# Performance work log

Measured on AMD Instinct MI355X. Metric: run time of the kernel, lower is better.

## Reference

```python
import jax, jax.numpy as jnp
import numpy as np

DIM = 64          # d_model
D_INNER = 128     # 2 * DIM (mamba expand=2)
D_STATE = 16
D_CONV = 4
DT_RANK = 4       # ceil(DIM / 16)


def setup_inputs() -> dict:
    key = jax.random.key(0)
    ks = jax.random.split(key, 8)
    s = 0.05
    f32 = jnp.float32
    return {
        "x": jax.random.normal(ks[0], (2, DIM, 96, 96), f32),
        # GroupNorm(1, dim)
        "gn_gamma": jnp.ones((DIM,), f32),
        "gn_beta": jnp.zeros((DIM,), f32),
        # Mamba params
        "W_in": (jax.random.normal(ks[1], (2 * D_INNER, DIM), f32) * s),
        "b_in": jnp.zeros((2 * D_INNER,), f32),
        "conv_w": (jax.random.normal(ks[2], (D_INNER, 1, D_CONV), f32) * s),
        "conv_b": jnp.zeros((D_INNER,), f32),
        "W_xproj": (jax.random.normal(ks[3], (DT_RANK + 2 * D_STATE, D_INNER), f32) * s),
        "W_dt": (jax.random.normal(ks[4], (D_INNER, DT_RANK), f32) * s),
        "b_dt": jnp.full((D_INNER,), -4.6, f32),  # softplus(-4.6) ~ 0.01
        "A_log": jnp.log(jnp.broadcast_to(jnp.arange(1, D_STATE + 1, dtype=f32), (D_INNER, D_STATE))),
        "Dp": jnp.ones((D_INNER,), f32),
        "W_out": (jax.random.normal(ks[5], (DIM, D_INNER), f32) * s),
        "b_out": jnp.zeros((DIM,), f32),
        # proj: Conv2d(dim, dim, 1) + BatchNorm2d(dim) eval-mode + GELU
        "proj_w": (jax.random.normal(ks[6], (DIM, DIM), f32) * s),
        "proj_b": jnp.zeros((DIM,), f32),
        "bn_gamma": jnp.ones((DIM,), f32),
        "bn_beta": jnp.zeros((DIM,), f32),
        "bn_mean": jnp.zeros((DIM,), f32),
        "bn_var": jnp.ones((DIM,), f32),
    }


def _mamba(u, W_in, b_in, conv_w, conv_b, W_xproj, W_dt, b_dt, A_log, Dp, W_out, b_out):
    # u: [B, L, DIM]
    xz = u @ W_in.T + b_in                      # [B, L, 2*D_INNER]
    x, z = jnp.split(xz, 2, axis=-1)            # each [B, L, D_INNER]
    # depthwise causal conv over L
    xc = jnp.transpose(x, (0, 2, 1))            # [B, D_INNER, L]
    xc = jax.lax.conv_general_dilated(
        xc, conv_w, (1,), [(D_CONV - 1, 0)],
        dimension_numbers=("NCH", "OIH", "NCH"), feature_group_count=D_INNER)
    x = jax.nn.silu(jnp.transpose(xc, (0, 2, 1)) + conv_b)   # [B, L, D_INNER]
    # input-dependent dt, B, C
    dbc = x @ W_xproj.T                          # [B, L, DT_RANK + 2*D_STATE]
    dt = dbc[..., :DT_RANK]
    Bm = dbc[..., DT_RANK:DT_RANK + D_STATE]     # [B, L, D_STATE]
    Cm = dbc[..., DT_RANK + D_STATE:]            # [B, L, D_STATE]
    dt = jax.nn.softplus(dt @ W_dt.T + b_dt)     # [B, L, D_INNER]
    A = -jnp.exp(A_log)                          # [D_INNER, D_STATE]
    deltaA = jnp.exp(dt[..., None] * A)                          # [B, L, D_INNER, D_STATE]
    deltaBu = dt[..., None] * Bm[:, :, None, :] * x[..., None]   # [B, L, D_INNER, D_STATE]
    # parallel linear recurrence h_t = a_t * h_{t-1} + b_t, h_0 = 0
    def comb(e1, e2):
        a1, b1 = e1
        a2, b2 = e2
        return a1 * a2, a2 * b1 + b2
    _, h = jax.lax.associative_scan(comb, (deltaA, deltaBu), axis=1)
    y = jnp.einsum("blds,bls->bld", h, Cm) + x * Dp
    y = y * jax.nn.silu(z)
    return y @ W_out.T + b_out                   # [B, L, DIM]


def reference(x, gn_gamma, gn_beta, W_in, b_in, conv_w, conv_b, W_xproj, W_dt, b_dt,
              A_log, Dp, W_out, b_out, proj_w, proj_b, bn_gamma, bn_beta, bn_mean, bn_var):
    B, C, H, W = x.shape
    # GroupNorm(1, C): normalize over (C, H, W) per sample, biased var
    mu = x.mean(axis=(1, 2, 3), keepdims=True)
    var = x.var(axis=(1, 2, 3), keepdims=True)
    xn = (x - mu) / jnp.sqrt(var + 1e-5)
    xn = xn * gn_gamma[None, :, None, None] + gn_beta[None, :, None, None]
    xn = jnp.clip(xn, -10.0, 10.0)
    res = xn
    seq = jnp.transpose(xn, (0, 2, 3, 1)).reshape(B, H * W, C)
    y = _mamba(seq, W_in, b_in, conv_w, conv_b, W_xproj, W_dt, b_dt, A_log, Dp, W_out, b_out)
    y2d = jnp.transpose(y.reshape(B, H, W, C), (0, 3, 1, 2))
    # proj: 1x1 conv + eval BatchNorm + exact GELU
    p = jnp.einsum("oc,bchw->bohw", proj_w, y2d) + proj_b[None, :, None, None]
    p = (p - bn_mean[None, :, None, None]) / jnp.sqrt(bn_var[None, :, None, None] + 1e-5)
    p = p * bn_gamma[None, :, None, None] + bn_beta[None, :, None, None]
    p = jax.nn.gelu(p, approximate=False)
    return jnp.clip(res + p, -10.0, 10.0)
```

## Files before the change

kernel.cpp:

```cpp
#include <hip/hip_runtime.h>
#include <math.h>

#define DIMC 64
#define DIN  128
#define LSEQ 9216
#define NPB  (DIMC*LSEQ)
#define NCH  192
#define CTL  48
#define NCHAIN 4096

__device__ __forceinline__ float siluf(float v)    { return v / (1.f + __expf(-v)); }
__device__ __forceinline__ float softplusf(float v){ return (v > 15.f) ? v : __logf(1.f + __expf(v)); }
__device__ __forceinline__ float clip10(float v)   { return fminf(10.f, fmaxf(-10.f, v)); }

__global__ void k_reduce(const float* __restrict__ x, float* __restrict__ sums) {
  int b = blockIdx.y;
  const float* xb = x + (size_t)b * NPB;
  float s = 0.f, s2 = 0.f;
  for (int i = blockIdx.x * blockDim.x + threadIdx.x; i < NPB; i += gridDim.x * blockDim.x) {
    float v = xb[i]; s += v; s2 = fmaf(v, v, s2);
  }
  __shared__ float l1[256], l2[256];
  int t = threadIdx.x;
  l1[t] = s; l2[t] = s2; __syncthreads();
  for (int off = 128; off > 0; off >>= 1) {
    if (t < off) { l1[t] += l1[t + off]; l2[t] += l2[t + off]; }
    __syncthreads();
  }
  if (t == 0) { atomicAdd(&sums[2*b], l1[0]); atomicAdd(&sums[2*b+1], l2[0]); }
}

__global__ void k_norm(const float* __restrict__ x, const float* __restrict__ gam,
                       const float* __restrict__ bet, const float* __restrict__ sums,
                       float* __restrict__ seq, float* __restrict__ res) {
  int b = blockIdx.y, l0 = blockIdx.x * 64;
  float mean = sums[2*b] * (1.f / NPB);
  float var  = sums[2*b+1] * (1.f / NPB) - mean * mean;
  float inv  = rsqrtf(var + 1e-5f);
  __shared__ float tile[64][65];
  int t = threadIdx.x;
  int lr = t & 63, cg = t >> 6;
  #pragma unroll
  for (int i = 0; i < 16; i++) {
    int c = i * 4 + cg;
    size_t idx = ((size_t)(b * DIMC + c)) * LSEQ + l0 + lr;
    float v = x[idx];
    v = (v - mean) * inv * gam[c] + bet[c];
    v = clip10(v);
    res[idx] = v;
    tile[c][lr] = v;
  }
  __syncthreads();
  int cc = t & 63, lg = t >> 6;
  #pragma unroll
  for (int i = 0; i < 16; i++) {
    int l = i * 4 + lg;
    seq[((size_t)(b * LSEQ + l0 + l)) * DIMC + cc] = tile[cc][l];
  }
}

__global__ void k_prep(const float* __restrict__ W_in, const float* __restrict__ proj_w,
                       const float* __restrict__ W_out, const float* __restrict__ b_out,
                       const float* __restrict__ proj_b, const float* __restrict__ W_xproj,
                       const float* __restrict__ W_dt,
                       float* __restrict__ Wt, float* __restrict__ Mt, float* __restrict__ bp,
                       float* __restrict__ Wbtd, float* __restrict__ Wbc) {
  int i = blockIdx.x * 256 + threadIdx.x;
  if (i < 16384) {
    int k = i >> 8, c = i & 255;
    Wt[i] = W_in[c * 64 + k];
    return;
  }
  int j = i - 16384;
  if (j < 8192) {
    int d = j >> 6, o = j & 63;
    float a = 0.f;
    for (int c = 0; c < 64; c++) a = fmaf(proj_w[o * 64 + c], W_out[c * DIN + d], a);
    Mt[j] = a;
    return;
  }
  int k2 = j - 8192;
  if (k2 < 64) {
    float a = proj_b[k2];
    for (int c = 0; c < 64; c++) a = fmaf(proj_w[k2 * 64 + c], b_out[c], a);
    bp[k2] = a;
    return;
  }
  int m = j - 8256;
  if (m < 16384) {
    int k = m >> 7, c = m & 127;
    float v = 0.f;
    #pragma unroll
    for (int r = 0; r < 4; r++) v = fmaf(W_dt[c * 4 + r], W_xproj[r * DIN + k], v);
    Wbtd[m] = v;
    return;
  }
  int m2 = m - 16384;
  if (m2 < 4096) {
    int k = m2 >> 5, jj = m2 & 31;
    Wbc[m2] = W_xproj[(4 + jj) * DIN + k];
  }
}

__global__ void __launch_bounds__(256) k_mid(
    const float* __restrict__ seq, const float* __restrict__ Wt,
    const float* __restrict__ b_in, const float* __restrict__ conv_w,
    const float* __restrict__ conv_b, const float* __restrict__ Wbtd,
    const float* __restrict__ Wbc, const float* __restrict__ b_dt,
    float* __restrict__ xs, float* __restrict__ zo, float* __restrict__ dt,
    float* __restrict__ Bm, float* __restrict__ Cm) {
  int row0 = blockIdx.x * 16;
  int l0 = row0 % LSEQ;
  int t = threadIdx.x;
  __shared__ float sq[19 * 64];
  __shared__ float xt[16 * DIN];
  for (int i = t; i < 19 * 16; i += 256) {
    int r = i >> 4, k4 = i & 15;
    int rr = row0 - 3 + r; if (rr < 0) rr = 0;
    *(float4*)(sq + r * 64 + k4 * 4) = *(const float4*)(seq + (size_t)rr * DIMC + k4 * 4);
  }
  __syncthreads();

  {
    int c = t;
    float bi = b_in[c];
    float a[19];
    #pragma unroll
    for (int r = 0; r < 19; r++) a[r] = bi;
    const float4* sq4 = (const float4*)sq;
    #pragma unroll 4
    for (int k4 = 0; k4 < 16; k4++) {
      float w0 = Wt[(k4 * 4 + 0) * 256 + c];
      float w1 = Wt[(k4 * 4 + 1) * 256 + c];
      float w2 = Wt[(k4 * 4 + 2) * 256 + c];
      float w3 = Wt[(k4 * 4 + 3) * 256 + c];
      #pragma unroll
      for (int r = 0; r < 19; r++) {
        float4 v = sq4[r * 16 + k4];
        a[r] = fmaf(w0, v.x, a[r]);
        a[r] = fmaf(w1, v.y, a[r]);
        a[r] = fmaf(w2, v.z, a[r]);
        a[r] = fmaf(w3, v.w, a[r]);
      }
    }
    if (c < DIN) {
      if (l0 == 0) { a[0] = 0.f; a[1] = 0.f; a[2] = 0.f; }
      float4 cw = *(const float4*)(conv_w + c * 4);
      float cb = conv_b[c];
      #pragma unroll
      for (int i = 0; i < 16; i++) {
        float v = cb;
        v = fmaf(a[i + 0], cw.x, v);
        v = fmaf(a[i + 1], cw.y, v);
        v = fmaf(a[i + 2], cw.z, v);
        v = fmaf(a[i + 3], cw.w, v);
        float sv = siluf(v);
        xs[(size_t)(row0 + i) * DIN + c] = sv;
        xt[i * DIN + c] = sv;
      }
    } else {
      int cz = c - DIN;
      #pragma unroll
      for (int i = 0; i < 16; i++) zo[(size_t)(row0 + i) * DIN + cz] = a[i + 3];
    }
  }
  __syncthreads();

  {
    int cd = t & 127, rb = (t >> 7) * 8;
    float acc[8];
    float bb = b_dt[cd];
    #pragma unroll
    for (int r = 0; r < 8; r++) acc[r] = bb;
    const float4* xt4 = (const float4*)(xt + rb * DIN);
    #pragma unroll 2
    for (int k4 = 0; k4 < 32; k4++) {
      float w0 = Wbtd[(k4 * 4 + 0) * 128 + cd];
      float w1 = Wbtd[(k4 * 4 + 1) * 128 + cd];
      float w2 = Wbtd[(k4 * 4 + 2) * 128 + cd];
      float w3 = Wbtd[(k4 * 4 + 3) * 128 + cd];
      #pragma unroll
      for (int r = 0; r < 8; r++) {
        float4 v = xt4[r * 32 + k4];
        acc[r] = fmaf(w0, v.x, acc[r]);
        acc[r] = fmaf(w1, v.y, acc[r]);
        acc[r] = fmaf(w2, v.z, acc[r]);
        acc[r] = fmaf(w3, v.w, acc[r]);
      }
    }
    #pragma unroll
    for (int r = 0; r < 8; r++)
      dt[(size_t)(row0 + rb + r) * DIN + cd] = softplusf(acc[r]);
  }

  {
    int cb = t & 31, rg = t >> 5;
    float a0 = 0.f, a1 = 0.f;
    const float4* x0 = (const float4*)(xt + (rg * 2 + 0) * DIN);
    const float4* x1 = (const float4*)(xt + (rg * 2 + 1) * DIN);
    #pragma unroll 2
    for (int k4 = 0; k4 < 32; k4++) {
      float w0 = Wbc[(k4 * 4 + 0) * 32 + cb];
      float w1 = Wbc[(k4 * 4 + 1) * 32 + cb];
      float w2 = Wbc[(k4 * 4 + 2) * 32 + cb];
      float w3 = Wbc[(k4 * 4 + 3) * 32 + cb];
      float4 v0 = x0[k4], v1 = x1[k4];
      a0 = fmaf(w0, v0.x, a0); a0 = fmaf(w1, v0.y, a0);
      a0 = fmaf(w2, v0.z, a0); a0 = fmaf(w3, v0.w, a0);
      a1 = fmaf(w0, v1.x, a1); a1 = fmaf(w1, v1.y, a1);
      a1 = fmaf(w2, v1.z, a1); a1 = fmaf(w3, v1.w, a1);
    }
    size_t r0 = (size_t)row0 + rg * 2;
    float* dst = (cb < 16) ? (Bm + r0 * 16 + cb) : (Cm + r0 * 16 + (cb - 16));
    dst[0]  = a0;
    dst[16] = a1;
  }
}

__global__ void __launch_bounds__(512) k_scanA(
    const float* __restrict__ dt, const float* __restrict__ Bmat,
    const float* __restrict__ xs, const float* __restrict__ A_log,
    float* __restrict__ Ap, float* __restrict__ Bg) {
  int chunk = blockIdx.x, b = blockIdx.y;
  int t = threadIdx.x;
  int d = t >> 2, q = t & 3;
  const float* al = A_log + d * 16 + q * 4;
  float a0 = -__expf(al[0]), a1 = -__expf(al[1]);
  float a2 = -__expf(al[2]), a3 = -__expf(al[3]);
  size_t base = (size_t)b * LSEQ + (size_t)chunk * CTL;
  const float* dtp = dt + base * DIN + d;
  const float* xsp = xs + base * DIN + d;
  const float4* bp4 = (const float4*)(Bmat + base * 16 + q * 4);
  float h0 = 0.f, h1 = 0.f, h2 = 0.f, h3 = 0.f;
  float p0 = 1.f, p1 = 1.f, p2 = 1.f, p3 = 1.f;
  #pragma unroll 4
  for (int i = 0; i < CTL; i++) {
    float dtv = dtp[(size_t)i * DIN];
    float xv  = xsp[(size_t)i * DIN];
    float4 bA = bp4[i * 4];
    float u = dtv * xv;
    float e;
    e = __expf(dtv * a0); h0 = fmaf(e, h0, u * bA.x); p0 *= e;
    e = __expf(dtv * a1); h1 = fmaf(e, h1, u * bA.y); p1 *= e;
    e = __expf(dtv * a2); h2 = fmaf(e, h2, u * bA.z); p2 *= e;
    e = __expf(dtv * a3); h3 = fmaf(e, h3, u * bA.w); p3 *= e;
  }
  size_t idx = (size_t)chunk * NCHAIN + (size_t)(b * DIN + d) * 16 + q * 4;
  *(float4*)(Ap + idx) = make_float4(p0, p1, p2, p3);
  *(float4*)(Bg + idx) = make_float4(h0, h1, h2, h3);
}

__global__ void k_scanB(const float* __restrict__ Ap, const float* __restrict__ Bg,
                        float* __restrict__ hinit) {
  int chain = blockIdx.x * 64 + threadIdx.x;
  float h = 0.f;
  for (int c = 0; c < NCH; c++) {
    size_t idx = (size_t)c * NCHAIN + chain;
    hinit[idx] = h;
    h = fmaf(Ap[idx], h, Bg[idx]);
  }
}

__global__ void __launch_bounds__(512) k_scanC(
    const float* __restrict__ dt, const float* __restrict__ Bmat,
    const float* __restrict__ Cmat, const float* __restrict__ xs,
    const float* __restrict__ z, const float* __restrict__ A_log,
    const float* __restrict__ Dp, const float* __restrict__ hinit,
    float* __restrict__ y) {
  int chunk = blockIdx.x, b = blockIdx.y;
  int t = threadIdx.x;
  int d = t >> 2, q = t & 3;
  const float* al = A_log + d * 16 + q * 4;
  float a0 = -__expf(al[0]), a1 = -__expf(al[1]);
  float a2 = -__expf(al[2]), a3 = -__expf(al[3]);
  float dp = Dp[d];
  size_t base = (size_t)b * LSEQ + (size_t)chunk * CTL;
  const float* dtp = dt + base * DIN + d;
  const float* xsp = xs + base * DIN + d;
  const float* zp  = z  + base * DIN + d;
  float* yp        = y  + base * DIN + d;
  const float4* bp4 = (const float4*)(Bmat + base * 16 + q * 4);
  const float4* cp4 = (const float4*)(Cmat + base * 16 + q * 4);
  size_t idx = (size_t)chunk * NCHAIN + (size_t)(b * DIN + d) * 16 + q * 4;
  float4 hv = *(const float4*)(hinit + idx);
  float h0 = hv.x, h1 = hv.y, h2 = hv.z, h3 = hv.w;
  #pragma unroll 2
  for (int i = 0; i < CTL; i++) {
    float dtv = dtp[(size_t)i * DIN];
    float xv  = xsp[(size_t)i * DIN];
    float4 bA = bp4[i * 4];
    float4 cA = cp4[i * 4];
    float u = dtv * xv;
    float e, p;
    e = __expf(dtv * a0); h0 = fmaf(e, h0, u * bA.x); p  = h0 * cA.x;
    e = __expf(dtv * a1); h1 = fmaf(e, h1, u * bA.y); p  = fmaf(h1, cA.y, p);
    e = __expf(dtv * a2); h2 = fmaf(e, h2, u * bA.z); p  = fmaf(h2, cA.z, p);
    e = __expf(dtv * a3); h3 = fmaf(e, h3, u * bA.w); p  = fmaf(h3, cA.w, p);
    p += __shfl_xor(p, 1);
    p += __shfl_xor(p, 2);
    if (q == 0) {
      float zv = zp[(size_t)i * DIN];
      yp[(size_t)i * DIN] = (p + xv * dp) * siluf(zv);
    }
  }
}

__global__ void __launch_bounds__(256) k_out(
    const float* __restrict__ y, const float* __restrict__ Mt,
    const float* __restrict__ bp, const float* __restrict__ bn_g,
    const float* __restrict__ bn_bt, const float* __restrict__ bn_m,
    const float* __restrict__ bn_v, const float* __restrict__ res,
    float* __restrict__ out) {
  int b = blockIdx.y, l0 = blockIdx.x * 32;
  int t = threadIdx.x;
  int c = t & 63, g = t >> 6;
  __shared__ float tile[64 * 33];
  float acc[8];
  float bpc = bp[c];
  #pragma unroll
  for (int i = 0; i < 8; i++) acc[i] = bpc;
  const float* yb = y + ((size_t)b * LSEQ + l0 + g * 8) * DIN;
  #pragma unroll 4
  for (int d4 = 0; d4 < 32; d4++) {
    float m0 = Mt[(d4 * 4 + 0) * 64 + c];
    float m1 = Mt[(d4 * 4 + 1) * 64 + c];
    float m2 = Mt[(d4 * 4 + 2) * 64 + c];
    float m3 = Mt[(d4 * 4 + 3) * 64 + c];
    #pragma unroll
    for (int i = 0; i < 8; i++) {
      float4 v = *(const float4*)(yb + (size_t)i * DIN + d4 * 4);
      acc[i] = fmaf(m0, v.x, acc[i]);
      acc[i] = fmaf(m1, v.y, acc[i]);
      acc[i] = fmaf(m2, v.z, acc[i]);
      acc[i] = fmaf(m3, v.w, acc[i]);
    }
  }
  float gg = bn_g[c], bt = bn_bt[c], mu = bn_m[c];
  float iv = rsqrtf(bn_v[c] + 1e-5f);
  #pragma unroll
  for (int i = 0; i < 8; i++) {
    float a = (acc[i] - mu) * iv * gg + bt;
    a = 0.5f * a * (1.f + erff(a * 0.70710678118654752f));
    tile[c * 33 + g * 8 + i] = a;
  }
  __syncthreads();
  int l = t & 31, cg = t >> 5;
  #pragma unroll
  for (int i = 0; i < 8; i++) {
    int cc = cg * 8 + i;
    size_t idx = ((size_t)(b * DIMC + cc)) * LSEQ + l0 + l;
    out[idx] = clip10(res[idx] + tile[cc * 33 + l]);
  }
}

extern "C" void kernel_launch(void* const* d_in, const int* in_sizes, int n_in,
                              void* d_out, int out_size, void* d_ws, size_t ws_size,
                              hipStream_t stream) {
  const float* x       = (const float*)d_in[0];
  const float* gn_g    = (const float*)d_in[1];
  const float* gn_b    = (const float*)d_in[2];
  const float* W_in    = (const float*)d_in[3];
  const float* b_in    = (const float*)d_in[4];
  const float* conv_w  = (const float*)d_in[5];
  const float* conv_b  = (const float*)d_in[6];
  const float* W_xproj = (const float*)d_in[7];
  const float* W_dt    = (const float*)d_in[8];
  const float* b_dt    = (const float*)d_in[9];
  const float* A_log   = (const float*)d_in[10];
  const float* Dp      = (const float*)d_in[11];
  const float* W_out   = (const float*)d_in[12];
  const float* b_out   = (const float*)d_in[13];
  const float* proj_w  = (const float*)d_in[14];
  const float* proj_b  = (const float*)d_in[15];
  const float* bn_g    = (const float*)d_in[16];
  const float* bn_bt   = (const float*)d_in[17];
  const float* bn_m    = (const float*)d_in[18];
  const float* bn_v    = (const float*)d_in[19];

  float* ws = (float*)d_ws;
  float* sums = ws;
  float* seq  = ws + 64;
  float* res  = seq + 1179648;
  float* ybuf = res + 1179648;
  float* zbuf = ybuf + 2359296;
  float* xsb  = zbuf + 2359296;
  float* dtb  = xsb + 2359296;
  float* Bmb  = dtb + 2359296;
  float* Cmb  = Bmb + 294912;
  float* Wt   = Cmb + 294912;
  float* Mt   = Wt + 16384;
  float* bp   = Mt + 8192;
  float* Wbtd = bp + 64;
  float* Wbc  = Wbtd + 16384;
  float* Bgb  = Wbc + 4096;
  float* hib  = Bgb + 786432;
  float* Apb  = seq;

  hipMemsetAsync(sums, 0, 64 * sizeof(float), stream);

  k_reduce<<<dim3(256, 2), 256, 0, stream>>>(x, sums);
  k_prep<<<177, 256, 0, stream>>>(W_in, proj_w, W_out, b_out, proj_b, W_xproj, W_dt,
                                  Wt, Mt, bp, Wbtd, Wbc);
  k_norm<<<dim3(144, 2), 256, 0, stream>>>(x, gn_g, gn_b, sums, seq, res);
  k_mid<<<1152, 256, 0, stream>>>(seq, Wt, b_in, conv_w, conv_b, Wbtd, Wbc, b_dt,
                                  xsb, zbuf, dtb, Bmb, Cmb);
  k_scanA<<<dim3(NCH, 2), 512, 0, stream>>>(dtb, Bmb, xsb, A_log, Apb, Bgb);
  k_scanB<<<64, 64, 0, stream>>>(Apb, Bgb, hib);
  k_scanC<<<dim3(NCH, 2), 512, 0, stream>>>(dtb, Bmb, Cmb, xsb, zbuf, A_log, Dp, hib, ybuf);
  k_out<<<dim3(288, 2), 256, 0, stream>>>(ybuf, Mt, bp, bn_g, bn_bt, bn_m, bn_v, res,
                                          (float*)d_out);
}
```

Baseline: 267.3 us.

## Fuse output projection into scan, merge reduce/prep, restructure mid GEMMs

Fuses the output projection, BatchNorm, GELU and residual clip into the final scan kernel, so y is kept in shared memory instead of being written to and read back from global memory. Merges the statistics reduction and weight-prep kernels into a single launch. Rewrites the in_proj part of k_mid to read seq directly from global memory with paired (x,z) float2 weights instead of staging it in shared memory, and repacks the dt and output weights into float2-interleaved layouts. The scan kernel gains more shared memory and registers, which may lower its occupancy.

```diff
diff --git a/kernel.cpp b/kernel.cpp
--- a/kernel.cpp
+++ b/kernel.cpp
@@ -12,22 +12,70 @@
 __device__ __forceinline__ float siluf(float v)    { return v / (1.f + __expf(-v)); }
 __device__ __forceinline__ float softplusf(float v){ return (v > 15.f) ? v : __logf(1.f + __expf(v)); }
 __device__ __forceinline__ float clip10(float v)   { return fminf(10.f, fmaxf(-10.f, v)); }
-
-__global__ void k_reduce(const float* __restrict__ x, float* __restrict__ sums) {
-  int b = blockIdx.y;
-  const float* xb = x + (size_t)b * NPB;
-  float s = 0.f, s2 = 0.f;
-  for (int i = blockIdx.x * blockDim.x + threadIdx.x; i < NPB; i += gridDim.x * blockDim.x) {
-    float v = xb[i]; s += v; s2 = fmaf(v, v, s2);
-  }
-  __shared__ float l1[256], l2[256];
+__device__ __forceinline__ float getc(const float4 v, int k) {
+  return (k == 0) ? v.x : (k == 1) ? v.y : (k == 2) ? v.z : v.w;
+}
+
+__global__ void k_init(const float* __restrict__ x, float* __restrict__ sums,
+                       const float* __restrict__ W_in, const float* __restrict__ proj_w,
+                       const float* __restrict__ W_out, const float* __restrict__ b_out,
+                       const float* __restrict__ proj_b, const float* __restrict__ W_xproj,
+                       const float* __restrict__ W_dt,
+                       float* __restrict__ Wtp, float* __restrict__ Mtp, float* __restrict__ bp,
+                       float* __restrict__ Wbtd2, float* __restrict__ Wbc) {
+  int bx = blockIdx.x, by = blockIdx.y;
   int t = threadIdx.x;
-  l1[t] = s; l2[t] = s2; __syncthreads();
-  for (int off = 128; off > 0; off >>= 1) {
-    if (t < off) { l1[t] += l1[t + off]; l2[t] += l2[t + off]; }
-    __syncthreads();
-  }
-  if (t == 0) { atomicAdd(&sums[2*b], l1[0]); atomicAdd(&sums[2*b+1], l2[0]); }
+  if (bx < 256) {
+    const float* xb = x + (size_t)by * NPB;
+    float s = 0.f, s2 = 0.f;
+    for (int i = bx * 256 + t; i < NPB; i += 65536) {
+      float v = xb[i]; s += v; s2 = fmaf(v, v, s2);
+    }
+    __shared__ float l1[256], l2[256];
+    l1[t] = s; l2[t] = s2; __syncthreads();
+    for (int off = 128; off > 0; off >>= 1) {
+      if (t < off) { l1[t] += l1[t + off]; l2[t] += l2[t + off]; }
+      __syncthreads();
+    }
+    if (t == 0) { atomicAdd(&sums[2*by], l1[0]); atomicAdd(&sums[2*by+1], l2[0]); }
+    return;
+  }
+  if (by != 0) return;
+  int i = (bx - 256) * 256 + t;
+  if (i < 16384) {
+    int k = i >> 8, cc = i & 255, c = cc & 127, h = cc >> 7;
+    Wtp[(k * 128 + c) * 2 + h] = W_in[(c + 128 * h) * 64 + k];
+    return;
+  }
+  int j = i - 16384;
+  if (j < 8192) {
+    int d = j >> 6, o = j & 63, o32 = o & 31, h = o >> 5;
+    float a = 0.f;
+    for (int c = 0; c < 64; c++) a = fmaf(proj_w[o * 64 + c], W_out[c * DIN + d], a);
+    Mtp[(d * 32 + o32) * 2 + h] = a;
+    return;
+  }
+  int k2 = j - 8192;
+  if (k2 < 64) {
+    float a = proj_b[k2];
+    for (int c = 0; c < 64; c++) a = fmaf(proj_w[k2 * 64 + c], b_out[c], a);
+    bp[k2] = a;
+    return;
+  }
+  int m = j - 8256;
+  if (m < 16384) {
+    int k = m >> 7, cc = m & 127, c = cc & 63, h = cc >> 6;
+    float v = 0.f;
+    #pragma unroll
+    for (int r = 0; r < 4; r++) v = fmaf(W_dt[(c + 64 * h) * 4 + r], W_xproj[r * DIN + k], v);
+    Wbtd2[(k * 64 + c) * 2 + h] = v;
+    return;
+  }
+  int m2 = m - 16384;
+  if (m2 < 4096) {
+    int k = m2 >> 5, jj = m2 & 31;
+    Wbc[m2] = W_xproj[(4 + jj) * DIN + k];
+  }
 }
 
 __global__ void k_norm(const float* __restrict__ x, const float* __restrict__ gam,
@@ -59,159 +107,111 @@
   }
 }
 
-__global__ void k_prep(const float* __restrict__ W_in, const float* __restrict__ proj_w,
-                       const float* __restrict__ W_out, const float* __restrict__ b_out,
-                       const float* __restrict__ proj_b, const float* __restrict__ W_xproj,
-                       const float* __restrict__ W_dt,
-                       float* __restrict__ Wt, float* __restrict__ Mt, float* __restrict__ bp,
-                       float* __restrict__ Wbtd, float* __restrict__ Wbc) {
-  int i = blockIdx.x * 256 + threadIdx.x;
-  if (i < 16384) {
-    int k = i >> 8, c = i & 255;
-    Wt[i] = W_in[c * 64 + k];
-    return;
-  }
-  int j = i - 16384;
-  if (j < 8192) {
-    int d = j >> 6, o = j & 63;
-    float a = 0.f;
-    for (int c = 0; c < 64; c++) a = fmaf(proj_w[o * 64 + c], W_out[c * DIN + d], a);
-    Mt[j] = a;
-    return;
-  }
-  int k2 = j - 8192;
-  if (k2 < 64) {
-    float a = proj_b[k2];
-    for (int c = 0; c < 64; c++) a = fmaf(proj_w[k2 * 64 + c], b_out[c], a);
-    bp[k2] = a;
-    return;
-  }
-  int m = j - 8256;
-  if (m < 16384) {
-    int k = m >> 7, c = m & 127;
-    float v = 0.f;
-    #pragma unroll
-    for (int r = 0; r < 4; r++) v = fmaf(W_dt[c * 4 + r], W_xproj[r * DIN + k], v);
-    Wbtd[m] = v;
-    return;
-  }
-  int m2 = m - 16384;
-  if (m2 < 4096) {
-    int k = m2 >> 5, jj = m2 & 31;
-    Wbc[m2] = W_xproj[(4 + jj) * DIN + k];
-  }
-}
-
 __global__ void __launch_bounds__(256) k_mid(
-    const float* __restrict__ seq, const float* __restrict__ Wt,
+    const float* __restrict__ seq, const float* __restrict__ Wtp,
     const float* __restrict__ b_in, const float* __restrict__ conv_w,
-    const float* __restrict__ conv_b, const float* __restrict__ Wbtd,
+    const float* __restrict__ conv_b, const float* __restrict__ Wbtd2,
     const float* __restrict__ Wbc, const float* __restrict__ b_dt,
     float* __restrict__ xs, float* __restrict__ zo, float* __restrict__ dt,
     float* __restrict__ Bm, float* __restrict__ Cm) {
   int row0 = blockIdx.x * 16;
-  int l0 = row0 % LSEQ;
   int t = threadIdx.x;
-  __shared__ float sq[19 * 64];
   __shared__ float xt[16 * DIN];
-  for (int i = t; i < 19 * 16; i += 256) {
-    int r = i >> 4, k4 = i & 15;
-    int rr = row0 - 3 + r; if (rr < 0) rr = 0;
-    *(float4*)(sq + r * 64 + k4 * 4) = *(const float4*)(seq + (size_t)rr * DIMC + k4 * 4);
+
+  {
+    int c = t & 127;
+    int rh = __builtin_amdgcn_readfirstlane(t >> 7);
+    long base = (long)row0 - 3 + rh * 8;
+    float bx_ = b_in[c], bz_ = b_in[c + 128];
+    float ax[11], az[11];
+    #pragma unroll
+    for (int j2 = 0; j2 < 11; j2++) { ax[j2] = bx_; az[j2] = bz_; }
+    const float4* sqg = (const float4*)seq;
+    const float2* W2  = (const float2*)Wtp;
+    for (int k4 = 0; k4 < 16; k4++) {
+      float4 sv[11];
+      #pragma unroll
+      for (int j2 = 0; j2 < 11; j2++) {
+        long rr = base + j2; if (rr < 0) rr = 0;
+        sv[j2] = sqg[(size_t)rr * 16 + k4];
+      }
+      #pragma unroll
+      for (int kk = 0; kk < 4; kk++) {
+        float2 w = W2[(size_t)(k4 * 4 + kk) * 128 + c];
+        #pragma unroll
+        for (int j2 = 0; j2 < 11; j2++) {
+          float svv = getc(sv[j2], kk);
+          ax[j2] = fmaf(w.x, svv, ax[j2]);
+          az[j2] = fmaf(w.y, svv, az[j2]);
+        }
+      }
+    }
+    if ((row0 % LSEQ) == 0 && rh == 0) { ax[0] = 0.f; ax[1] = 0.f; ax[2] = 0.f; }
+    float4 cw = *(const float4*)(conv_w + c * 4);
+    float cb = conv_b[c];
+    #pragma unroll
+    for (int i2 = 0; i2 < 8; i2++) {
+      float v = cb;
+      v = fmaf(ax[i2 + 0], cw.x, v);
+      v = fmaf(ax[i2 + 1], cw.y, v);
+      v = fmaf(ax[i2 + 2], cw.z, v);
+      v = fmaf(ax[i2 + 3], cw.w, v);
+      float sv_ = siluf(v);
+      int r = rh * 8 + i2;
+      xs[(size_t)(row0 + r) * DIN + c] = sv_;
+      xt[r * DIN + c] = sv_;
+      zo[(size_t)(row0 + r) * DIN + c] = az[i2 + 3];
+    }
   }
   __syncthreads();
 
+  const float4* xt4 = (const float4*)xt;
+
   {
-    int c = t;
-    float bi = b_in[c];
-    float a[19];
-    #pragma unroll
-    for (int r = 0; r < 19; r++) a[r] = bi;
-    const float4* sq4 = (const float4*)sq;
-    #pragma unroll 4
-    for (int k4 = 0; k4 < 16; k4++) {
-      float w0 = Wt[(k4 * 4 + 0) * 256 + c];
-      float w1 = Wt[(k4 * 4 + 1) * 256 + c];
-      float w2 = Wt[(k4 * 4 + 2) * 256 + c];
-      float w3 = Wt[(k4 * 4 + 3) * 256 + c];
+    int cd = t & 63, rg = t >> 6;
+    float acc0[4], acc1[4];
+    float bd0 = b_dt[cd], bd1 = b_dt[cd + 64];
+    #pragma unroll
+    for (int r = 0; r < 4; r++) { acc0[r] = bd0; acc1[r] = bd1; }
+    const float2* Wd2 = (const float2*)Wbtd2;
+    for (int k4 = 0; k4 < 32; k4++) {
+      float4 v0 = xt4[(rg * 4 + 0) * 32 + k4];
+      float4 v1 = xt4[(rg * 4 + 1) * 32 + k4];
+      float4 v2 = xt4[(rg * 4 + 2) * 32 + k4];
+      float4 v3 = xt4[(rg * 4 + 3) * 32 + k4];
       #pragma unroll
-      for (int r = 0; r < 19; r++) {
-        float4 v = sq4[r * 16 + k4];
-        a[r] = fmaf(w0, v.x, a[r]);
-        a[r] = fmaf(w1, v.y, a[r]);
-        a[r] = fmaf(w2, v.z, a[r]);
-        a[r] = fmaf(w3, v.w, a[r]);
-      }
-    }
-    if (c < DIN) {
-      if (l0 == 0) { a[0] = 0.f; a[1] = 0.f; a[2] = 0.f; }
-      float4 cw = *(const float4*)(conv_w + c * 4);
-      float cb = conv_b[c];
+      for (int kk = 0; kk < 4; kk++) {
+        float2 w = Wd2[(size_t)(k4 * 4 + kk) * 64 + cd];
+        float s0 = getc(v0, kk), s1 = getc(v1, kk), s2 = getc(v2, kk), s3 = getc(v3, kk);
+        acc0[0] = fmaf(w.x, s0, acc0[0]); acc1[0] = fmaf(w.y, s0, acc1[0]);
+        acc0[1] = fmaf(w.x, s1, acc0[1]); acc1[1] = fmaf(w.y, s1, acc1[1]);
+        acc0[2] = fmaf(w.x, s2, acc0[2]); acc1[2] = fmaf(w.y, s2, acc1[2]);
+        acc0[3] = fmaf(w.x, s3, acc0[3]); acc1[3] = fmaf(w.y, s3, acc1[3]);
+      }
+    }
+    #pragma unroll
+    for (int r = 0; r < 4; r++) {
+      size_t ro = (size_t)(row0 + rg * 4 + r) * DIN;
+      dt[ro + cd]      = softplusf(acc0[r]);
+      dt[ro + cd + 64] = softplusf(acc1[r]);
+    }
+  }
+
+  {
+    int cb2 = t & 31, rg = t >> 5;
+    float a0 = 0.f, a1 = 0.f;
+    for (int k4 = 0; k4 < 32; k4++) {
+      float4 v0 = xt4[(rg * 2 + 0) * 32 + k4];
+      float4 v1 = xt4[(rg * 2 + 1) * 32 + k4];
       #pragma unroll
-      for (int i = 0; i < 16; i++) {
-        float v = cb;
-        v = fmaf(a[i + 0], cw.x, v);
-        v = fmaf(a[i + 1], cw.y, v);
-        v = fmaf(a[i + 2], cw.z, v);
-        v = fmaf(a[i + 3], cw.w, v);
-        float sv = siluf(v);
-        xs[(size_t)(row0 + i) * DIN + c] = sv;
-        xt[i * DIN + c] = sv;
-      }
-    } else {
-      int cz = c - DIN;
-      #pragma unroll
-      for (int i = 0; i < 16; i++) zo[(size_t)(row0 + i) * DIN + cz] = a[i + 3];
-    }
-  }
-  __syncthreads();
-
-  {
-    int cd = t & 127, rb = (t >> 7) * 8;
-    float acc[8];
-    float bb = b_dt[cd];
-    #pragma unroll
-    for (int r = 0; r < 8; r++) acc[r] = bb;
-    const float4* xt4 = (const float4*)(xt + rb * DIN);
-    #pragma unroll 2
-    for (int k4 = 0; k4 < 32; k4++) {
-      float w0 = Wbtd[(k4 * 4 + 0) * 128 + cd];
-      float w1 = Wbtd[(k4 * 4 + 1) * 128 + cd];
-      float w2 = Wbtd[(k4 * 4 + 2) * 128 + cd];
-      float w3 = Wbtd[(k4 * 4 + 3) * 128 + cd];
-      #pragma unroll
-      for (int r = 0; r < 8; r++) {
-        float4 v = xt4[r * 32 + k4];
-        acc[r] = fmaf(w0, v.x, acc[r]);
-        acc[r] = fmaf(w1, v.y, acc[r]);
-        acc[r] = fmaf(w2, v.z, acc[r]);
-        acc[r] = fmaf(w3, v.w, acc[r]);
-      }
-    }
-    #pragma unroll
-    for (int r = 0; r < 8; r++)
-      dt[(size_t)(row0 + rb + r) * DIN + cd] = softplusf(acc[r]);
-  }
-
-  {
-    int cb = t & 31, rg = t >> 5;
-    float a0 = 0.f, a1 = 0.f;
-    const float4* x0 = (const float4*)(xt + (rg * 2 + 0) * DIN);
-    const float4* x1 = (const float4*)(xt + (rg * 2 + 1) * DIN);
-    #pragma unroll 2
-    for (int k4 = 0; k4 < 32; k4++) {
-      float w0 = Wbc[(k4 * 4 + 0) * 32 + cb];
-      float w1 = Wbc[(k4 * 4 + 1) * 32 + cb];
-      float w2 = Wbc[(k4 * 4 + 2) * 32 + cb];
-      float w3 = Wbc[(k4 * 4 + 3) * 32 + cb];
-      float4 v0 = x0[k4], v1 = x1[k4];
-      a0 = fmaf(w0, v0.x, a0); a0 = fmaf(w1, v0.y, a0);
-      a0 = fmaf(w2, v0.z, a0); a0 = fmaf(w3, v0.w, a0);
-      a1 = fmaf(w0, v1.x, a1); a1 = fmaf(w1, v1.y, a1);
-      a1 = fmaf(w2, v1.z, a1); a1 = fmaf(w3, v1.w, a1);
+      for (int kk = 0; kk < 4; kk++) {
+        float w = Wbc[(k4 * 4 + kk) * 32 + cb2];
+        a0 = fmaf(w, getc(v0, kk), a0);
+        a1 = fmaf(w, getc(v1, kk), a1);
+      }
     }
     size_t r0 = (size_t)row0 + rg * 2;
-    float* dst = (cb < 16) ? (Bm + r0 * 16 + cb) : (Cm + r0 * 16 + (cb - 16));
+    float* dst = (cb2 < 16) ? (Bm + r0 * 16 + cb2) : (Cm + r0 * 16 + (cb2 - 16));
     dst[0]  = a0;
     dst[16] = a1;
   }
@@ -266,90 +266,102 @@
     const float* __restrict__ Cmat, const float* __restrict__ xs,
     const float* __restrict__ z, const float* __restrict__ A_log,
     const float* __restrict__ Dp, const float* __restrict__ hinit,
-    float* __restrict__ y) {
+    const float* __restrict__ Mtp, const float* __restrict__ bp,
+    const float* __restrict__ bn_g, const float* __restrict__ bn_bt,
+    const float* __restrict__ bn_m, const float* __restrict__ bn_v,
+    const float* __restrict__ res, float* __restrict__ out) {
   int chunk = blockIdx.x, b = blockIdx.y;
   int t = threadIdx.x;
-  int d = t >> 2, q = t & 3;
-  const float* al = A_log + d * 16 + q * 4;
-  float a0 = -__expf(al[0]), a1 = -__expf(al[1]);
-  float a2 = -__expf(al[2]), a3 = -__expf(al[3]);
-  float dp = Dp[d];
-  size_t base = (size_t)b * LSEQ + (size_t)chunk * CTL;
-  const float* dtp = dt + base * DIN + d;
-  const float* xsp = xs + base * DIN + d;
-  const float* zp  = z  + base * DIN + d;
-  float* yp        = y  + base * DIN + d;
-  const float4* bp4 = (const float4*)(Bmat + base * 16 + q * 4);
-  const float4* cp4 = (const float4*)(Cmat + base * 16 + q * 4);
-  size_t idx = (size_t)chunk * NCHAIN + (size_t)(b * DIN + d) * 16 + q * 4;
-  float4 hv = *(const float4*)(hinit + idx);
-  float h0 = hv.x, h1 = hv.y, h2 = hv.z, h3 = hv.w;
-  #pragma unroll 2
-  for (int i = 0; i < CTL; i++) {
-    float dtv = dtp[(size_t)i * DIN];
-    float xv  = xsp[(size_t)i * DIN];
-    float4 bA = bp4[i * 4];
-    float4 cA = cp4[i * 4];
-    float u = dtv * xv;
-    float e, p;
-    e = __expf(dtv * a0); h0 = fmaf(e, h0, u * bA.x); p  = h0 * cA.x;
-    e = __expf(dtv * a1); h1 = fmaf(e, h1, u * bA.y); p  = fmaf(h1, cA.y, p);
-    e = __expf(dtv * a2); h2 = fmaf(e, h2, u * bA.z); p  = fmaf(h2, cA.z, p);
-    e = __expf(dtv * a3); h3 = fmaf(e, h3, u * bA.w); p  = fmaf(h3, cA.w, p);
-    p += __shfl_xor(p, 1);
-    p += __shfl_xor(p, 2);
-    if (q == 0) {
-      float zv = zp[(size_t)i * DIN];
-      yp[(size_t)i * DIN] = (p + xv * dp) * siluf(zv);
-    }
-  }
-}
-
-__global__ void __launch_bounds__(256) k_out(
-    const float* __restrict__ y, const float* __restrict__ Mt,
-    const float* __restrict__ bp, const float* __restrict__ bn_g,
-    const float* __restrict__ bn_bt, const float* __restrict__ bn_m,
-    const float* __restrict__ bn_v, const float* __restrict__ res,
-    float* __restrict__ out) {
-  int b = blockIdx.y, l0 = blockIdx.x * 32;
-  int t = threadIdx.x;
-  int c = t & 63, g = t >> 6;
-  __shared__ float tile[64 * 33];
-  float acc[8];
-  float bpc = bp[c];
-  #pragma unroll
-  for (int i = 0; i < 8; i++) acc[i] = bpc;
-  const float* yb = y + ((size_t)b * LSEQ + l0 + g * 8) * DIN;
-  #pragma unroll 4
-  for (int d4 = 0; d4 < 32; d4++) {
-    float m0 = Mt[(d4 * 4 + 0) * 64 + c];
-    float m1 = Mt[(d4 * 4 + 1) * 64 + c];
-    float m2 = Mt[(d4 * 4 + 2) * 64 + c];
-    float m3 = Mt[(d4 * 4 + 3) * 64 + c];
-    #pragma unroll
-    for (int i = 0; i < 8; i++) {
-      float4 v = *(const float4*)(yb + (size_t)i * DIN + d4 * 4);
-      acc[i] = fmaf(m0, v.x, acc[i]);
-      acc[i] = fmaf(m1, v.y, acc[i]);
-      acc[i] = fmaf(m2, v.z, acc[i]);
-      acc[i] = fmaf(m3, v.w, acc[i]);
-    }
-  }
-  float gg = bn_g[c], bt = bn_bt[c], mu = bn_m[c];
-  float iv = rsqrtf(bn_v[c] + 1e-5f);
-  #pragma unroll
-  for (int i = 0; i < 8; i++) {
-    float a = (acc[i] - mu) * iv * gg + bt;
-    a = 0.5f * a * (1.f + erff(a * 0.70710678118654752f));
-    tile[c * 33 + g * 8 + i] = a;
+  __shared__ float ytile[CTL * DIN];
+  __shared__ float trans[64 * 52];
+  {
+    int d = t >> 2, q = t & 3;
+    const float* al = A_log + d * 16 + q * 4;
+    float a0 = -__expf(al[0]), a1 = -__expf(al[1]);
+    float a2 = -__expf(al[2]), a3 = -__expf(al[3]);
+    float dp = Dp[d];
+    size_t base = (size_t)b * LSEQ + (size_t)chunk * CTL;
+    const float* dtp = dt + base * DIN + d;
+    const float* xsp = xs + base * DIN + d;
+    const float* zp  = z  + base * DIN + d;
+    const float4* bp4 = (const float4*)(Bmat + base * 16 + q * 4);
+    const float4* cp4 = (const float4*)(Cmat + base * 16 + q * 4);
+    size_t idx = (size_t)chunk * NCHAIN + (size_t)(b * DIN + d) * 16 + q * 4;
+    float4 hv = *(const float4*)(hinit + idx);
+    float h0 = hv.x, h1 = hv.y, h2 = hv.z, h3 = hv.w;
+    #pragma unroll 2
+    for (int i = 0; i < CTL; i++) {
+      float dtv = dtp[(size_t)i * DIN];
+      float xv  = xsp[(size_t)i * DIN];
+      float4 bA = bp4[i * 4];
+      float4 cA = cp4[i * 4];
+      float u = dtv * xv;
+      float e, p;
+      e = __expf(dtv * a0); h0 = fmaf(e, h0, u * bA.x); p = h0 * cA.x;
+      e = __expf(dtv * a1); h1 = fmaf(e, h1, u * bA.y); p = fmaf(h1, cA.y, p);
+      e = __expf(dtv * a2); h2 = fmaf(e, h2, u * bA.z); p = fmaf(h2, cA.z, p);
+      e = __expf(dtv * a3); h3 = fmaf(e, h3, u * bA.w); p = fmaf(h3, cA.w, p);
+      p += __shfl_xor(p, 1);
+      p += __shfl_xor(p, 2);
+      if (q == 0) {
+        float zv = zp[(size_t)i * DIN];
+        ytile[i * DIN + d] = (p + xv * dp) * siluf(zv);
+      }
+    }
   }
   __syncthreads();
-  int l = t & 31, cg = t >> 5;
-  #pragma unroll
-  for (int i = 0; i < 8; i++) {
-    int cc = cg * 8 + i;
-    size_t idx = ((size_t)(b * DIMC + cc)) * LSEQ + l0 + l;
-    out[idx] = clip10(res[idx] + tile[cc * 33 + l]);
+
+  {
+    int op = t & 31, rg = t >> 5;
+    float acc0[3], acc1[3];
+    float b0 = bp[op], b1 = bp[op + 32];
+    #pragma unroll
+    for (int r = 0; r < 3; r++) { acc0[r] = b0; acc1[r] = b1; }
+    const float4* yt4 = (const float4*)ytile;
+    const float2* M2  = (const float2*)Mtp;
+    for (int k4 = 0; k4 < 32; k4++) {
+      float4 v0 = yt4[(rg * 3 + 0) * 32 + k4];
+      float4 v1 = yt4[(rg * 3 + 1) * 32 + k4];
+      float4 v2 = yt4[(rg * 3 + 2) * 32 + k4];
+      #pragma unroll
+      for (int kk = 0; kk < 4; kk++) {
+        float2 w = M2[(size_t)(k4 * 4 + kk) * 32 + op];
+        float s0 = getc(v0, kk), s1 = getc(v1, kk), s2 = getc(v2, kk);
+        acc0[0] = fmaf(w.x, s0, acc0[0]); acc1[0] = fmaf(w.y, s0, acc1[0]);
+        acc0[1] = fmaf(w.x, s1, acc0[1]); acc1[1] = fmaf(w.y, s1, acc1[1]);
+        acc0[2] = fmaf(w.x, s2, acc0[2]); acc1[2] = fmaf(w.y, s2, acc1[2]);
+      }
+    }
+    float g0 = bn_g[op], bt0 = bn_bt[op], mu0 = bn_m[op];
+    float iv0 = rsqrtf(bn_v[op] + 1e-5f);
+    float g1 = bn_g[op + 32], bt1 = bn_bt[op + 32], mu1 = bn_m[op + 32];
+    float iv1 = rsqrtf(bn_v[op + 32] + 1e-5f);
+    __syncthreads();
+    #pragma unroll
+    for (int r = 0; r < 3; r++) {
+      int row = rg * 3 + r;
+      float a = (acc0[r] - mu0) * iv0 * g0 + bt0;
+      a = 0.5f * a * (1.f + erff(a * 0.70710678118654752f));
+      trans[op * 52 + row] = a;
+      float a2 = (acc1[r] - mu1) * iv1 * g1 + bt1;
+      a2 = 0.5f * a2 * (1.f + erff(a2 * 0.70710678118654752f));
+      trans[(op + 32) * 52 + row] = a2;
+    }
+  }
+  __syncthreads();
+
+  int l0c = chunk * CTL;
+  for (int task = t; task < 768; task += 512) {
+    int c = task / 12, f = task - c * 12;
+    float4 vv = *(const float4*)(trans + c * 52 + f * 4);
+    size_t gi = ((size_t)(b * DIMC + c)) * LSEQ + l0c + f * 4;
+    const float4 rv = *(const float4*)(res + gi);
+    float4 o;
+    o.x = clip10(rv.x + vv.x);
+    o.y = clip10(rv.y + vv.y);
+    o.z = clip10(rv.z + vv.z);
+    o.w = clip10(rv.w + vv.w);
+    *(float4*)(out + gi) = o;
   }
 }
 
@@ -381,32 +393,30 @@
   float* sums = ws;
   float* seq  = ws + 64;
   float* res  = seq + 1179648;
-  float* ybuf = res + 1179648;
-  float* zbuf = ybuf + 2359296;
+  float* zbuf = res + 1179648;
   float* xsb  = zbuf + 2359296;
   float* dtb  = xsb + 2359296;
   float* Bmb  = dtb + 2359296;
   float* Cmb  = Bmb + 294912;
-  float* Wt   = Cmb + 294912;
-  float* Mt   = Wt + 16384;
-  float* bp   = Mt + 8192;
-  float* Wbtd = bp + 64;
-  float* Wbc  = Wbtd + 16384;
+  float* Wtp  = Cmb + 294912;
+  float* Mtp  = Wtp + 16384;
+  float* bp   = Mtp + 8192;
+  float* Wbtd2= bp + 64;
+  float* Wbc  = Wbtd2 + 16384;
   float* Bgb  = Wbc + 4096;
   float* hib  = Bgb + 786432;
   float* Apb  = seq;
 
   hipMemsetAsync(sums, 0, 64 * sizeof(float), stream);
 
-  k_reduce<<<dim3(256, 2), 256, 0, stream>>>(x, sums);
-  k_prep<<<177, 256, 0, stream>>>(W_in, proj_w, W_out, b_out, proj_b, W_xproj, W_dt,
-                                  Wt, Mt, bp, Wbtd, Wbc);
+  k_init<<<dim3(433, 2), 256, 0, stream>>>(x, sums, W_in, proj_w, W_out, b_out, proj_b,
+                                           W_xproj, W_dt, Wtp, Mtp, bp, Wbtd2, Wbc);
   k_norm<<<dim3(144, 2), 256, 0, stream>>>(x, gn_g, gn_b, sums, seq, res);
-  k_mid<<<1152, 256, 0, stream>>>(seq, Wt, b_in, conv_w, conv_b, Wbtd, Wbc, b_dt,
+  k_mid<<<1152, 256, 0, stream>>>(seq, Wtp, b_in, conv_w, conv_b, Wbtd2, Wbc, b_dt,
                                   xsb, zbuf, dtb, Bmb, Cmb);
   k_scanA<<<dim3(NCH, 2), 512, 0, stream>>>(dtb, Bmb, xsb, A_log, Apb, Bgb);
   k_scanB<<<64, 64, 0, stream>>>(Apb, Bgb, hib);
-  k_scanC<<<dim3(NCH, 2), 512, 0, stream>>>(dtb, Bmb, Cmb, xsb, zbuf, A_log, Dp, hib, ybuf);
-  k_out<<<dim3(288, 2), 256, 0, stream>>>(ybuf, Mt, bp, bn_g, bn_bt, bn_m, bn_v, res,
-                                          (float*)d_out);
-}
+  k_scanC<<<dim3(NCH, 2), 512, 0, stream>>>(dtb, Bmb, Cmb, xsb, zbuf, A_log, Dp, hib,
+                                            Mtp, bp, bn_g, bn_bt, bn_m, bn_v, res,
+                                            (float*)d_out);
+}
```

Result: faster. 248.7 us (-7.0%).
